# Kernel tuning notes

Hardware: AMD Instinct MI355X
Metric: run time of the kernel (lower is better)

Reference implementation:

```python
import jax, jax.numpy as jnp
import numpy as np

L, B, S, D = 4, 32, 512, 64  # labels, batch, seq_len (nodes), embed_dim
EDGE_P = 0.05                # adjacency density


def setup_inputs() -> dict:
    key = jax.random.key(0)
    ks = jax.random.split(key, 8)
    gcn_in = jax.random.normal(ks[0], (B, S, D), jnp.float32)
    # bool relational adjacency [L, B, S, S]; sparse-ish like real dependency/semantic graphs
    adj_mat = jax.random.bernoulli(ks[1], EDGE_P, (L, B, S, S))
    num_words = jnp.full((B,), float(S - 1), jnp.float32)
    eye = jnp.eye(D, dtype=jnp.float32)
    # weights initialized as identity (per tf.eye init) plus small noise so grads/outputs are non-trivial
    W_in = eye[None] + 0.05 * jax.random.normal(ks[2], (L, D, D), jnp.float32)
    W_out = eye[None] + 0.05 * jax.random.normal(ks[3], (L, D, D), jnp.float32)
    b_in = jnp.zeros((L, D), jnp.float32)
    b_out = jnp.zeros((L, D), jnp.float32)
    Wg_in = 0.05 * jax.random.normal(ks[4], (L, D), jnp.float32)
    Wg_out = 0.05 * jax.random.normal(ks[5], (L, D), jnp.float32)
    bg_in = jnp.zeros((L,), jnp.float32)
    bg_out = jnp.zeros((L,), jnp.float32)
    return {"gcn_in": gcn_in, "adj_mat": adj_mat, "num_words": num_words,
            "W_in": W_in, "b_in": b_in, "Wg_in": Wg_in, "bg_in": bg_in,
            "W_out": W_out, "b_out": b_out, "Wg_out": Wg_out, "bg_out": bg_out}


def reference(gcn_in, adj_mat, num_words, W_in, b_in, Wg_in, bg_in,
              W_out, b_out, Wg_out, bg_out):
    """RFGCN gcnLayer, 1 layer, aggregate='sum', w_gating=True, dropout off.

    All L relation labels are batched into single einsums instead of a
    Python loop over labels (same math, vectorized).
    """
    adj = adj_mat.astype(jnp.float32)  # [L,B,S,S], adj[l,b,src,dst]

    # self-loop: w_loop is a fixed identity -> loop_act == gcn_in
    act_sum = gcn_in  # [B,S,D]

    # ---- in-arcs: aggregate with adj^T (adj[l] transposed on last two dims) ----
    inp_in = jnp.einsum('bsd,lde->lbse', gcn_in, W_in) + b_in[:, None, None, :]
    # in_t[l,b,i] = sum_j adj[l,b,j,i] * inp_in[l,b,j]
    in_t = jnp.einsum('lbji,lbje->lbie', adj, inp_in)
    gin = jnp.einsum('bsd,ld->lbs', gcn_in, Wg_in) + bg_in[:, None, None]
    in_gate = jnp.einsum('lbji,lbj->lbi', adj, gin)
    in_act = in_t * jax.nn.sigmoid(in_gate)[..., None]

    # ---- out-arcs: aggregate with adj[l] directly ----
    inp_out = jnp.einsum('bsd,lde->lbse', gcn_in, W_out) + b_out[:, None, None, :]
    # out_t[l,b,i] = sum_j adj[l,b,i,j] * inp_out[l,b,j]
    out_t = jnp.einsum('lbij,lbje->lbie', adj, inp_out)
    gout = jnp.einsum('bsd,ld->lbs', gcn_in, Wg_out) + bg_out[:, None, None]
    out_gate = jnp.einsum('lbij,lbj->lbi', adj, gout)
    out_act = out_t * jax.nn.sigmoid(out_gate)[..., None]

    act_sum = act_sum + jnp.sum(in_act + out_act, axis=0)  # sum over labels
    act_sum = act_sum / (3.0 * num_words)[:, None, None]
    # single layer => last layer => no ReLU (relu applied only when layer != last)
    return act_sum
```

## Files before the change

### kernel.cpp

```cpp
#include <hip/hip_runtime.h>
#include <math.h>

typedef short short8 __attribute__((ext_vector_type(8)));
typedef float f32x4  __attribute__((ext_vector_type(4)));

constexpr int Ssz = 512, Dsz = 64, Lsz = 4, Bsz = 32;
constexpr int TI = 32, TJ = 64;

constexpr size_t XBF_OFF = 0;
constexpr size_t RM_OFF  = 2u * 1024 * 1024;
constexpr size_t CM_OFF  = RM_OFF + 4u * 1024 * 1024;
constexpr size_t WS_NEED = CM_OFF + 4u * 1024 * 1024;

constexpr int YBs = 69;
constexpr int YB_f = 0;
constexpr int WBs = 68;
constexpr int WB_f = YB_f + 32 * YBs;
constexpr int DG_f = WB_f + 64 * WBs;
constexpr int WG_f = DG_f + 32;
constexpr int BB_f = WG_f + 64;
constexpr int EPI_FLOATS = BB_f + 64;

__device__ __forceinline__ unsigned short f2bf(float x) {
    union { float f; unsigned u; } v; v.f = x;
    unsigned r = v.u + 0x7FFFu + ((v.u >> 16) & 1u);
    return (unsigned short)(r >> 16);
}

__global__ __launch_bounds__(256)
void xpose_kernel(const float* __restrict__ X, unsigned short* __restrict__ xbf)
{
    __shared__ unsigned short t[64][66];
    const int b = blockIdx.y, s0 = blockIdx.x * 64;
    const int tid = threadIdx.x;
    const int c = tid & 63, r4 = tid >> 6;
    const float* Xb = X + (size_t)b * Ssz * Dsz;
#pragma unroll
    for (int k = 0; k < 16; ++k) {
        const int s = r4 + 4 * k;
        t[s][c] = f2bf(Xb[(size_t)(s0 + s) * Dsz + c]);
    }
    __syncthreads();
    unsigned short* o = xbf + (size_t)b * Dsz * Ssz;
#pragma unroll
    for (int k = 0; k < 16; ++k) {
        const int d = r4 + 4 * k;
        o[(size_t)d * Ssz + s0 + c] = t[c][d];
    }
}

__global__ __launch_bounds__(256)
void mask_kernel(const int* __restrict__ adj,
                 unsigned long long* __restrict__ rm,
                 unsigned long long* __restrict__ cm)
{
    const int tid  = threadIdx.x;
    const int lane = tid & 63;
    const int wt   = blockIdx.x * 4 + (tid >> 6);
    const int lb   = wt >> 6;
    const int rem  = wt & 63;
    const int r1t  = (rem >> 3) * 64;
    const int r2t  = (rem & 7) * 64;
    const int* A = adj + (size_t)lb * Ssz * Ssz;

    unsigned long long c = 0ull, rmine = 0ull;
#pragma unroll 4
    for (int j = 0; j < 64; ++j) {
        const int a = A[(size_t)(r1t + j) * Ssz + r2t + lane];
        const unsigned long long bal = __ballot(a != 0);
        if (lane == j) rmine = bal;
        c |= ((unsigned long long)(a != 0)) << j;
    }
    rm[((size_t)lb * 8 + (r2t >> 6)) * 512 + r1t + lane] = rmine;
    cm[((size_t)lb * 8 + (r1t >> 6)) * 512 + r2t + lane] = c;
}

__global__ __launch_bounds__(512, 2)
void rfgcn_main(const float* __restrict__ X,
                const unsigned short* __restrict__ xbf,
                const unsigned long long* __restrict__ rm,
                const unsigned long long* __restrict__ cm,
                const float* __restrict__ nw,
                const float* __restrict__ W_in,  const float* __restrict__ b_in,
                const float* __restrict__ wg_in, const float* __restrict__ bg_in,
                const float* __restrict__ W_out, const float* __restrict__ b_out,
                const float* __restrict__ wg_out,const float* __restrict__ bg_out,
                float* __restrict__ out)
{
    __shared__ float smf[EPI_FLOATS];

    const int tid  = threadIdx.x;
    const int b    = blockIdx.y;
    const int i0   = blockIdx.x * TI;
    const int w    = tid >> 6;
    const int lane = tid & 63;
    const int dir  = w & 1;
    const int wl   = w >> 1;
    const int lm   = lane & 15;
    const int lg   = lane >> 4;

    f32x4 acc[2][4];
    f32x4 dacc[2];
#pragma unroll
    for (int rt = 0; rt < 2; ++rt) {
#pragma unroll
        for (int nt = 0; nt < 4; ++nt) acc[rt][nt] = (f32x4){0.f, 0.f, 0.f, 0.f};
        dacc[rt] = (f32x4){0.f, 0.f, 0.f, 0.f};
    }
    const short8 ones = {(short)0x3F80, (short)0x3F80, (short)0x3F80, (short)0x3F80,
                         (short)0x3F80, (short)0x3F80, (short)0x3F80, (short)0x3F80};

    const unsigned long long* Mb = (dir ? rm : cm) + (size_t)(wl * Bsz + b) * 8 * 512;
    const unsigned short* xp0 = xbf + (size_t)b * Dsz * Ssz;

    for (int jc = 0; jc < 8; ++jc) {
        const unsigned long long m0 = Mb[(size_t)jc * 512 + i0 + lm];
        const unsigned long long m1 = Mb[(size_t)jc * 512 + i0 + 16 + lm];
        const unsigned short* xp = xp0 + jc * 64;
#pragma unroll
        for (int ks = 0; ks < 2; ++ks) {
            short8 bh[4];
#pragma unroll
            for (int nt = 0; nt < 4; ++nt)
                bh[nt] = *(const short8*)(xp + (size_t)(16 * nt + lm) * Ssz + 8 * (4 * ks + lg));
#pragma unroll
            for (int rt = 0; rt < 2; ++rt) {
                const unsigned bytev = (unsigned)((rt ? m1 : m0) >> (32 * ks + 8 * lg)) & 0xFFu;
                short8 af;
#pragma unroll
                for (int jj = 0; jj < 8; ++jj)
                    af[jj] = ((bytev >> jj) & 1u) ? (short)0x3F80 : (short)0;
#pragma unroll
                for (int nt = 0; nt < 4; ++nt)
                    acc[rt][nt] = __builtin_amdgcn_mfma_f32_16x16x32_bf16(af, bh[nt], acc[rt][nt], 0, 0, 0);
                dacc[rt] = __builtin_amdgcn_mfma_f32_16x16x32_bf16(af, ones, dacc[rt], 0, 0, 0);
            }
        }
    }

    const int ei  = tid & 31;
    const int ecg = tid >> 5;
    float fin[4];
#pragma unroll
    for (int q = 0; q < 4; ++q) fin[q] = 0.f;

#pragma unroll
    for (int l = 0; l < Lsz; ++l) {
#pragma unroll
        for (int d2 = 0; d2 < 2; ++d2) {
            __syncthreads();
            if (dir == d2 && wl == l) {
#pragma unroll
                for (int rt = 0; rt < 2; ++rt)
#pragma unroll
                    for (int nt = 0; nt < 4; ++nt)
#pragma unroll
                        for (int r = 0; r < 4; ++r)
                            smf[YB_f + (16 * rt + 4 * lg + r) * YBs + nt * 16 + lm] = acc[rt][nt][r];
                if (lm == 0)
#pragma unroll
                    for (int rt = 0; rt < 2; ++rt)
#pragma unroll
                        for (int r = 0; r < 4; ++r)
                            smf[DG_f + 16 * rt + 4 * lg + r] = dacc[rt][r];
            }
            const float* Wp = (d2 ? W_out : W_in) + l * Dsz * Dsz;
            {
                const int r = tid >> 3, c8 = tid & 7;
                *(float4*)&smf[WB_f + r * WBs + 8 * c8]     = *(const float4*)&Wp[r * Dsz + 8 * c8];
                *(float4*)&smf[WB_f + r * WBs + 8 * c8 + 4] = *(const float4*)&Wp[r * Dsz + 8 * c8 + 4];
            }
            const float* wgp = (d2 ? wg_out : wg_in) + l * Dsz;
            const float* bp  = (d2 ? b_out  : b_in)  + l * Dsz;
            if (tid < 64)        smf[WG_f + tid]      = wgp[tid];
            else if (tid < 128)  smf[BB_f + tid - 64] = bp[tid - 64];
            const float bgs = (d2 ? bg_out : bg_in)[l];
            __syncthreads();

            const float dg = smf[DG_f + ei];
            float tq[4];
#pragma unroll
            for (int q = 0; q < 4; ++q) tq[q] = dg * smf[BB_f + 4 * ecg + q];
            float gate = dg * bgs;
#pragma unroll 4
            for (int e = 0; e < 64; ++e) {
                const float yv = smf[YB_f + ei * YBs + e];
                gate += yv * smf[WG_f + e];
#pragma unroll
                for (int q = 0; q < 4; ++q) tq[q] += yv * smf[WB_f + e * WBs + 4 * ecg + q];
            }
            const float sg = 1.f / (1.f + expf(-gate));
#pragma unroll
            for (int q = 0; q < 4; ++q) fin[q] += tq[q] * sg;
        }
    }

    const float inv = 1.f / (3.f * nw[b]);
    const float* Xb = X + (size_t)b * Ssz * Dsz;
    const float4 xr = *(const float4*)&Xb[(size_t)(i0 + ei) * Dsz + 4 * ecg];
    float4 o;
    o.x = (xr.x + fin[0]) * inv;
    o.y = (xr.y + fin[1]) * inv;
    o.z = (xr.z + fin[2]) * inv;
    o.w = (xr.w + fin[3]) * inv;
    *(float4*)(out + ((size_t)b * Ssz + i0 + ei) * Dsz + 4 * ecg) = o;
}

constexpr int XTb[2] = {0, 4096};
constexpr int FB_SMEM = EPI_FLOATS * 4;

__global__ __launch_bounds__(512, 4)
void rfgcn_fallback(const float* __restrict__ X, const int* __restrict__ adj,
                    const float* __restrict__ nw,
                    const float* __restrict__ W_in,  const float* __restrict__ b_in,
                    const float* __restrict__ wg_in, const float* __restrict__ bg_in,
                    const float* __restrict__ W_out, const float* __restrict__ b_out,
                    const float* __restrict__ wg_out,const float* __restrict__ bg_out,
                    float* __restrict__ out)
{
    __shared__ __align__(16) char smem[FB_SMEM];
    short* sm16 = (short*)smem;
    float* smf  = (float*)smem;

    const int tid  = threadIdx.x;
    const int b    = blockIdx.y;
    const int i0   = blockIdx.x * TI;
    const int w    = tid >> 6;
    const int lane = tid & 63;
    const int dir  = w & 1;
    const int wl   = w >> 1;
    const int lm   = lane & 15;
    const int lg   = lane >> 4;

    f32x4 acc[2][4];
    f32x4 dacc[2];
#pragma unroll
    for (int rt = 0; rt < 2; ++rt) {
#pragma unroll
        for (int nt = 0; nt < 4; ++nt) acc[rt][nt] = (f32x4){0.f, 0.f, 0.f, 0.f};
        dacc[rt] = (f32x4){0.f, 0.f, 0.f, 0.f};
    }
    const short8 ones = {(short)0x3F80, (short)0x3F80, (short)0x3F80, (short)0x3F80,
                         (short)0x3F80, (short)0x3F80, (short)0x3F80, (short)0x3F80};

    const float* Xb = X + (size_t)b * Ssz * Dsz;
    const int*   Ab = adj + ((size_t)wl * Bsz + b) * Ssz * Ssz;

    float xv[8];
    int   aR[32];

#define ADJ_LOAD(T)                                                              \
    {                                                                            \
        const int J0 = (T) * TJ;                                                 \
        if (dir == 0) {                                                          \
            _Pragma("unroll")                                                    \
            for (int rt = 0; rt < 2; ++rt)                                       \
                _Pragma("unroll")                                                \
                for (int ks = 0; ks < 2; ++ks)                                   \
                    _Pragma("unroll")                                            \
                    for (int j = 0; j < 8; ++j)                                  \
                        aR[rt * 16 + ks * 8 + j] =                               \
                            Ab[(size_t)(J0 + 32 * ks + 8 * lg + j) * Ssz + i0 + 16 * rt + lm]; \
        } else {                                                                 \
            _Pragma("unroll")                                                    \
            for (int rt = 0; rt < 2; ++rt)                                       \
                _Pragma("unroll")                                                \
                for (int ks = 0; ks < 2; ++ks) {                                 \
                    const int* p = &Ab[(size_t)(i0 + 16 * rt + lm) * Ssz + J0 + 32 * ks + 8 * lg]; \
                    const int4 q0 = *(const int4*)p;                             \
                    const int4 q1 = *(const int4*)(p + 4);                       \
                    aR[rt * 16 + ks * 8 + 0] = q0.x; aR[rt * 16 + ks * 8 + 1] = q0.y; \
                    aR[rt * 16 + ks * 8 + 2] = q0.z; aR[rt * 16 + ks * 8 + 3] = q0.w; \
                    aR[rt * 16 + ks * 8 + 4] = q1.x; aR[rt * 16 + ks * 8 + 5] = q1.y; \
                    aR[rt * 16 + ks * 8 + 6] = q1.z; aR[rt * 16 + ks * 8 + 7] = q1.w; \
                }                                                                \
        }                                                                        \
    }
#define X_LOAD(T)                                                                \
    {                                                                            \
        const int J0 = (T) * TJ;                                                 \
        _Pragma("unroll")                                                        \
        for (int s = 0; s < 8; ++s) xv[s] = Xb[(size_t)(J0 + 8 * w + s) * Dsz + lane]; \
    }
#define X_WRITE(BUF)                                                             \
    {                                                                            \
        short8 hi;                                                               \
        _Pragma("unroll")                                                        \
        for (int s = 0; s < 8; ++s) hi[s] = (short)f2bf(xv[s]);                  \
        const int g = w ^ (lane & 7);                                            \
        *(short8*)(sm16 + XTb[BUF] + lane * 64 + g * 8) = hi;                    \
    }

    X_LOAD(0)
    X_WRITE(0)
    ADJ_LOAD(0)
    X_LOAD(1)
    __syncthreads();

    for (int t = 0; t < 8; ++t) {
        const int cur = t & 1;
        short8 af[2][2];
#pragma unroll
        for (int rt = 0; rt < 2; ++rt)
#pragma unroll
            for (int ks = 0; ks < 2; ++ks)
#pragma unroll
                for (int j = 0; j < 8; ++j)
                    af[rt][ks][j] = aR[rt * 16 + ks * 8 + j] ? (short)0x3F80 : (short)0;

        if (t < 7) ADJ_LOAD(t + 1)
        if (t < 7) X_WRITE(cur ^ 1)
        if (t < 6) X_LOAD(t + 2)

#pragma unroll
        for (int ks = 0; ks < 2; ++ks) {
            short8 bh[4];
#pragma unroll
            for (int nt = 0; nt < 4; ++nt) {
                const int d = nt * 16 + lm;
                const int g = (4 * ks + lg) ^ (d & 7);
                bh[nt] = *(const short8*)(sm16 + XTb[cur] + d * 64 + g * 8);
            }
#pragma unroll
            for (int rt = 0; rt < 2; ++rt) {
#pragma unroll
                for (int nt = 0; nt < 4; ++nt)
                    acc[rt][nt] = __builtin_amdgcn_mfma_f32_16x16x32_bf16(af[rt][ks], bh[nt], acc[rt][nt], 0, 0, 0);
                dacc[rt] = __builtin_amdgcn_mfma_f32_16x16x32_bf16(af[rt][ks], ones, dacc[rt], 0, 0, 0);
            }
        }
        __syncthreads();
    }
#undef ADJ_LOAD
#undef X_LOAD
#undef X_WRITE

    const int ei  = tid & 31;
    const int ecg = tid >> 5;
    float fin[4];
#pragma unroll
    for (int q = 0; q < 4; ++q) fin[q] = 0.f;

#pragma unroll
    for (int l = 0; l < Lsz; ++l) {
#pragma unroll
        for (int d2 = 0; d2 < 2; ++d2) {
            if (l + d2) __syncthreads();
            if (dir == d2 && wl == l) {
#pragma unroll
                for (int rt = 0; rt < 2; ++rt)
#pragma unroll
                    for (int nt = 0; nt < 4; ++nt)
#pragma unroll
                        for (int r = 0; r < 4; ++r)
                            smf[YB_f + (16 * rt + 4 * lg + r) * YBs + nt * 16 + lm] = acc[rt][nt][r];
                if (lm == 0)
#pragma unroll
                    for (int rt = 0; rt < 2; ++rt)
#pragma unroll
                        for (int r = 0; r < 4; ++r)
                            smf[DG_f + 16 * rt + 4 * lg + r] = dacc[rt][r];
            }
            const float* Wp = (d2 ? W_out : W_in) + l * Dsz * Dsz;
            {
                const int r = tid >> 3, c8 = tid & 7;
                *(float4*)&smf[WB_f + r * WBs + 8 * c8]     = *(const float4*)&Wp[r * Dsz + 8 * c8];
                *(float4*)&smf[WB_f + r * WBs + 8 * c8 + 4] = *(const float4*)&Wp[r * Dsz + 8 * c8 + 4];
            }
            const float* wgp = (d2 ? wg_out : wg_in) + l * Dsz;
            const float* bp  = (d2 ? b_out  : b_in)  + l * Dsz;
            if (tid < 64)        smf[WG_f + tid]      = wgp[tid];
            else if (tid < 128)  smf[BB_f + tid - 64] = bp[tid - 64];
            const float bgs = (d2 ? bg_out : bg_in)[l];
            __syncthreads();

            const float dg = smf[DG_f + ei];
            float tq[4];
#pragma unroll
            for (int q = 0; q < 4; ++q) tq[q] = dg * smf[BB_f + 4 * ecg + q];
            float gate = dg * bgs;
#pragma unroll 4
            for (int e = 0; e < 64; ++e) {
                const float yv = smf[YB_f + ei * YBs + e];
                gate += yv * smf[WG_f + e];
#pragma unroll
                for (int q = 0; q < 4; ++q) tq[q] += yv * smf[WB_f + e * WBs + 4 * ecg + q];
            }
            const float sg = 1.f / (1.f + expf(-gate));
#pragma unroll
            for (int q = 0; q < 4; ++q) fin[q] += tq[q] * sg;
        }
    }

    const float inv = 1.f / (3.f * nw[b]);
    const float4 xr = *(const float4*)&Xb[(size_t)(i0 + ei) * Dsz + 4 * ecg];
    float4 o;
    o.x = (xr.x + fin[0]) * inv;
    o.y = (xr.y + fin[1]) * inv;
    o.z = (xr.z + fin[2]) * inv;
    o.w = (xr.w + fin[3]) * inv;
    *(float4*)(out + ((size_t)b * Ssz + i0 + ei) * Dsz + 4 * ecg) = o;
}

extern "C" void kernel_launch(void* const* d_in, const int* in_sizes, int n_in,
                              void* d_out, int out_size, void* d_ws, size_t ws_size,
                              hipStream_t stream)
{
    const float* X      = (const float*)d_in[0];
    const int*   adj    = (const int*)  d_in[1];
    const float* nw     = (const float*)d_in[2];
    const float* W_in   = (const float*)d_in[3];
    const float* b_in   = (const float*)d_in[4];
    const float* wg_in  = (const float*)d_in[5];
    const float* bg_in  = (const float*)d_in[6];
    const float* W_out  = (const float*)d_in[7];
    const float* b_out  = (const float*)d_in[8];
    const float* wg_out = (const float*)d_in[9];
    const float* bg_out = (const float*)d_in[10];
    float* out = (float*)d_out;

    if (ws_size >= WS_NEED) {
        unsigned short*      xbf = (unsigned short*)((char*)d_ws + XBF_OFF);
        unsigned long long*  rmp = (unsigned long long*)((char*)d_ws + RM_OFF);
        unsigned long long*  cmp = (unsigned long long*)((char*)d_ws + CM_OFF);
        hipLaunchKernelGGL(xpose_kernel, dim3(8, 32), dim3(256), 0, stream, X, xbf);
        hipLaunchKernelGGL(mask_kernel, dim3(2048), dim3(256), 0, stream, adj, rmp, cmp);
        hipLaunchKernelGGL(rfgcn_main, dim3(Ssz / TI, Bsz), dim3(512), 0, stream,
                           X, xbf, rmp, cmp, nw, W_in, b_in, wg_in, bg_in,
                           W_out, b_out, wg_out, bg_out, out);
    } else {
        hipLaunchKernelGGL(rfgcn_fallback, dim3(Ssz / TI, Bsz), dim3(512), 0, stream,
                           X, adj, nw, W_in, b_in, wg_in, bg_in,
                           W_out, b_out, wg_out, bg_out, out);
    }
}
```

Baseline: 92.07 us.

## Run per-label epilogue projection on MFMA in parallel across warps

The epilogue used to loop serially over the 8 (label, direction) pairs, with a block-wide sync and a scalar FP32 64x64 projection for each. Now every warp stages its own aggregated tile as bf16 in swizzled LDS and projects it with MFMA against bf16-converted W, with the gate weights as an extra column tile. Results are summed into a shared buffer through LDS atomics. This removes 16 barriers and the scalar FMA loop, and launch bounds are raised to 4 blocks per CU, at the cost of rounding the intermediate and the weights to bf16 and reading weights uncoalesced from global memory.

```diff
diff --git a/kernel.cpp b/kernel.cpp
--- a/kernel.cpp
+++ b/kernel.cpp
@@ -11,6 +11,11 @@
 constexpr size_t RM_OFF  = 2u * 1024 * 1024;
 constexpr size_t CM_OFF  = RM_OFF + 4u * 1024 * 1024;
 constexpr size_t WS_NEED = CM_OFF + 4u * 1024 * 1024;
+
+constexpr int YS_B   = 0;
+constexpr int DEG_B2 = 32768;
+constexpr int FIN_B2 = DEG_B2 + 1024;
+constexpr int MAIN_SMEM = FIN_B2 + 8448;
 
 constexpr int YBs = 69;
 constexpr int YB_f = 0;
@@ -75,7 +80,7 @@
     cm[((size_t)lb * 8 + (r1t >> 6)) * 512 + r2t + lane] = c;
 }
 
-__global__ __launch_bounds__(512, 2)
+__global__ __launch_bounds__(512, 4)
 void rfgcn_main(const float* __restrict__ X,
                 const unsigned short* __restrict__ xbf,
                 const unsigned long long* __restrict__ rm,
@@ -87,7 +92,10 @@
                 const float* __restrict__ wg_out,const float* __restrict__ bg_out,
                 float* __restrict__ out)
 {
-    __shared__ float smf[EPI_FLOATS];
+    __shared__ __align__(16) char smem[MAIN_SMEM];
+    short* sm16 = (short*)smem;
+    float* degf = (float*)(smem + DEG_B2);
+    float* finf = (float*)(smem + FIN_B2);
 
     const int tid  = threadIdx.x;
     const int b    = blockIdx.y;
@@ -99,6 +107,8 @@
     const int lm   = lane & 15;
     const int lg   = lane >> 4;
 
+    for (int k = tid; k < 64 * 33; k += 512) finf[k] = 0.f;
+
     f32x4 acc[2][4];
     f32x4 dacc[2];
 #pragma unroll
@@ -138,72 +148,103 @@
         }
     }
 
-    const int ei  = tid & 31;
-    const int ecg = tid >> 5;
-    float fin[4];
-#pragma unroll
-    for (int q = 0; q < 4; ++q) fin[q] = 0.f;
-
-#pragma unroll
-    for (int l = 0; l < Lsz; ++l) {
-#pragma unroll
-        for (int d2 = 0; d2 < 2; ++d2) {
-            __syncthreads();
-            if (dir == d2 && wl == l) {
-#pragma unroll
-                for (int rt = 0; rt < 2; ++rt)
-#pragma unroll
-                    for (int nt = 0; nt < 4; ++nt)
-#pragma unroll
-                        for (int r = 0; r < 4; ++r)
-                            smf[YB_f + (16 * rt + 4 * lg + r) * YBs + nt * 16 + lm] = acc[rt][nt][r];
-                if (lm == 0)
-#pragma unroll
-                    for (int rt = 0; rt < 2; ++rt)
-#pragma unroll
-                        for (int r = 0; r < 4; ++r)
-                            smf[DG_f + 16 * rt + 4 * lg + r] = dacc[rt][r];
-            }
-            const float* Wp = (d2 ? W_out : W_in) + l * Dsz * Dsz;
-            {
-                const int r = tid >> 3, c8 = tid & 7;
-                *(float4*)&smf[WB_f + r * WBs + 8 * c8]     = *(const float4*)&Wp[r * Dsz + 8 * c8];
-                *(float4*)&smf[WB_f + r * WBs + 8 * c8 + 4] = *(const float4*)&Wp[r * Dsz + 8 * c8 + 4];
-            }
-            const float* wgp = (d2 ? wg_out : wg_in) + l * Dsz;
-            const float* bp  = (d2 ? b_out  : b_in)  + l * Dsz;
-            if (tid < 64)        smf[WG_f + tid]      = wgp[tid];
-            else if (tid < 128)  smf[BB_f + tid - 64] = bp[tid - 64];
-            const float bgs = (d2 ? bg_out : bg_in)[l];
-            __syncthreads();
-
-            const float dg = smf[DG_f + ei];
-            float tq[4];
-#pragma unroll
-            for (int q = 0; q < 4; ++q) tq[q] = dg * smf[BB_f + 4 * ecg + q];
-            float gate = dg * bgs;
-#pragma unroll 4
-            for (int e = 0; e < 64; ++e) {
-                const float yv = smf[YB_f + ei * YBs + e];
-                gate += yv * smf[WG_f + e];
-#pragma unroll
-                for (int q = 0; q < 4; ++q) tq[q] += yv * smf[WB_f + e * WBs + 4 * ecg + q];
-            }
-            const float sg = 1.f / (1.f + expf(-gate));
-#pragma unroll
-            for (int q = 0; q < 4; ++q) fin[q] += tq[q] * sg;
-        }
-    }
+    short* Ys = sm16 + YS_B / 2 + w * 2048;
+#pragma unroll
+    for (int rt = 0; rt < 2; ++rt)
+#pragma unroll
+        for (int nt = 0; nt < 4; ++nt)
+#pragma unroll
+            for (int r = 0; r < 4; ++r) {
+                const int row = 16 * rt + 4 * lg + r;
+                const int gs  = (((2 * nt + (lm >> 3)) ^ (row & 7)) << 3) + (lm & 7);
+                Ys[row * 64 + gs] = (short)f2bf(acc[rt][nt][r]);
+            }
+    if (lm == 0) {
+#pragma unroll
+        for (int rt = 0; rt < 2; ++rt)
+#pragma unroll
+            for (int r = 0; r < 4; ++r)
+                degf[w * 32 + 16 * rt + 4 * lg + r] = dacc[rt][r];
+    }
+
+    short8 by[2][2];
+#pragma unroll
+    for (int it = 0; it < 2; ++it)
+#pragma unroll
+        for (int ks = 0; ks < 2; ++ks) {
+            const int i  = 16 * it + lm;
+            const int gs = ((lg + 4 * ks) ^ (i & 7)) << 3;
+            by[it][ks] = *(const short8*)(Ys + i * 64 + gs);
+        }
+    float degv[2];
+#pragma unroll
+    for (int it = 0; it < 2; ++it) degv[it] = degf[w * 32 + 16 * it + lm];
+
+    const float* Wp  = (dir ? W_out  : W_in)  + wl * Dsz * Dsz;
+    const float* wgp = (dir ? wg_out : wg_in) + wl * Dsz;
+    const float* bp  = (dir ? b_out  : b_in)  + wl * Dsz;
+    const float  bgv = (dir ? bg_out : bg_in)[wl];
+
+    f32x4 accT[5][2];
+#pragma unroll
+    for (int ct = 0; ct < 5; ++ct)
+#pragma unroll
+        for (int it = 0; it < 2; ++it) accT[ct][it] = (f32x4){0.f, 0.f, 0.f, 0.f};
+
+#pragma unroll
+    for (int ct = 0; ct < 5; ++ct) {
+#pragma unroll
+        for (int ks = 0; ks < 2; ++ks) {
+            short8 aw;
+            if (ct < 4) {
+                const int c = 16 * ct + lm;
+#pragma unroll
+                for (int j = 0; j < 8; ++j)
+                    aw[j] = (short)f2bf(Wp[(size_t)(8 * lg + j + 32 * ks) * Dsz + c]);
+            } else {
+#pragma unroll
+                for (int j = 0; j < 8; ++j)
+                    aw[j] = (short)f2bf(wgp[8 * lg + j + 32 * ks]);
+            }
+#pragma unroll
+            for (int it = 0; it < 2; ++it)
+                accT[ct][it] = __builtin_amdgcn_mfma_f32_16x16x32_bf16(aw, by[it][ks], accT[ct][it], 0, 0, 0);
+        }
+    }
+
+    float sg[2];
+#pragma unroll
+    for (int it = 0; it < 2; ++it) {
+        const float g = accT[4][it][0] + degv[it] * bgv;
+        sg[it] = 1.f / (1.f + expf(-g));
+    }
+    __syncthreads();
+#pragma unroll
+    for (int ct = 0; ct < 4; ++ct)
+#pragma unroll
+        for (int r = 0; r < 4; ++r) {
+            const int c = 16 * ct + 4 * lg + r;
+            const float bc = bp[c];
+#pragma unroll
+            for (int it = 0; it < 2; ++it) {
+                const float v = (accT[ct][it][r] + degv[it] * bc) * sg[it];
+                atomicAdd(&finf[c * 33 + 16 * it + lm], v);
+            }
+        }
+
+    __syncthreads();
 
     const float inv = 1.f / (3.f * nw[b]);
     const float* Xb = X + (size_t)b * Ssz * Dsz;
-    const float4 xr = *(const float4*)&Xb[(size_t)(i0 + ei) * Dsz + 4 * ecg];
+    const int oi = tid >> 4;
+    const int c4 = (tid & 15) * 4;
+    const float4 xv = *(const float4*)&Xb[(size_t)(i0 + oi) * Dsz + c4];
     float4 o;
-    o.x = (xr.x + fin[0]) * inv;
-    o.y = (xr.y + fin[1]) * inv;
-    o.z = (xr.z + fin[2]) * inv;
-    o.w = (xr.w + fin[3]) * inv;
-    *(float4*)(out + ((size_t)b * Ssz + i0 + ei) * Dsz + 4 * ecg) = o;
+    o.x = (xv.x + finf[(c4 + 0) * 33 + oi]) * inv;
+    o.y = (xv.y + finf[(c4 + 1) * 33 + oi]) * inv;
+    o.z = (xv.z + finf[(c4 + 2) * 33 + oi]) * inv;
+    o.w = (xv.w + finf[(c4 + 3) * 33 + oi]) * inv;
+    *(float4*)(out + ((size_t)b * Ssz + i0 + oi) * Dsz + c4) = o;
 }
 
 constexpr int XTb[2] = {0, 4096};
```

Result: slower. 108.7 us (+18.1%).

## Split fused aggregation/epilogue kernel into separate MFMA aggregation and epilogue kernels

Applied to the files above, without the earlier changes.

The fused main kernel is split in two. A 64-thread agg_kernel, launched per (tile, batch, label*direction), computes the masked aggregation and degree with MFMA and writes them to a global workspace. A separate epi_kernel then streams each aggregate into LDS and applies the weight projection, gating and sum. The aim is more independent blocks for the aggregation phase and lighter epilogue blocks with higher occupancy. In exchange, roughly 32MB of intermediate fp32 data makes a round trip through global memory, and there is one more kernel launch.

```diff
diff --git a/kernel.cpp b/kernel.cpp
--- a/kernel.cpp
+++ b/kernel.cpp
@@ -8,9 +8,11 @@
 constexpr int TI = 32, TJ = 64;
 
 constexpr size_t XBF_OFF = 0;
-constexpr size_t RM_OFF  = 2u * 1024 * 1024;
-constexpr size_t CM_OFF  = RM_OFF + 4u * 1024 * 1024;
-constexpr size_t WS_NEED = CM_OFF + 4u * 1024 * 1024;
+constexpr size_t RM_OFF  = 2u  * 1024 * 1024;
+constexpr size_t CM_OFF  = 6u  * 1024 * 1024;
+constexpr size_t Y_OFF   = 10u * 1024 * 1024;
+constexpr size_t D_OFF   = 42u * 1024 * 1024;
+constexpr size_t WS_NEED = D_OFF + 512u * 1024;
 
 constexpr int YBs = 69;
 constexpr int YB_f = 0;
@@ -75,11 +77,81 @@
     cm[((size_t)lb * 8 + (r1t >> 6)) * 512 + r2t + lane] = c;
 }
 
-__global__ __launch_bounds__(512, 2)
-void rfgcn_main(const float* __restrict__ X,
-                const unsigned short* __restrict__ xbf,
+__global__ __launch_bounds__(64, 4)
+void agg_kernel(const unsigned short* __restrict__ xbf,
                 const unsigned long long* __restrict__ rm,
                 const unsigned long long* __restrict__ cm,
+                float* __restrict__ Yws, float* __restrict__ Dws)
+{
+    const int ix   = blockIdx.x;
+    const int b    = blockIdx.y;
+    const int dirl = blockIdx.z;
+    const int dir  = dirl & 1, wl = dirl >> 1;
+    const int lane = threadIdx.x;
+    const int lm   = lane & 15;
+    const int lg   = lane >> 4;
+    const int i0   = ix * TI;
+
+    f32x4 acc[2][4];
+    f32x4 dacc[2];
+#pragma unroll
+    for (int rt = 0; rt < 2; ++rt) {
+#pragma unroll
+        for (int nt = 0; nt < 4; ++nt) acc[rt][nt] = (f32x4){0.f, 0.f, 0.f, 0.f};
+        dacc[rt] = (f32x4){0.f, 0.f, 0.f, 0.f};
+    }
+    const short8 ones = {(short)0x3F80, (short)0x3F80, (short)0x3F80, (short)0x3F80,
+                         (short)0x3F80, (short)0x3F80, (short)0x3F80, (short)0x3F80};
+
+    const unsigned long long* Mb = (dir ? rm : cm) + (size_t)(wl * Bsz + b) * 8 * 512;
+    const unsigned short* xp0 = xbf + (size_t)b * Dsz * Ssz;
+
+    for (int jc = 0; jc < 8; ++jc) {
+        const unsigned long long m0 = Mb[(size_t)jc * 512 + i0 + lm];
+        const unsigned long long m1 = Mb[(size_t)jc * 512 + i0 + 16 + lm];
+        const unsigned short* xp = xp0 + jc * 64;
+#pragma unroll
+        for (int ks = 0; ks < 2; ++ks) {
+            short8 bh[4];
+#pragma unroll
+            for (int nt = 0; nt < 4; ++nt)
+                bh[nt] = *(const short8*)(xp + (size_t)(16 * nt + lm) * Ssz + 8 * (4 * ks + lg));
+#pragma unroll
+            for (int rt = 0; rt < 2; ++rt) {
+                const unsigned bytev = (unsigned)((rt ? m1 : m0) >> (32 * ks + 8 * lg)) & 0xFFu;
+                short8 af;
+#pragma unroll
+                for (int jj = 0; jj < 8; ++jj)
+                    af[jj] = ((bytev >> jj) & 1u) ? (short)0x3F80 : (short)0;
+#pragma unroll
+                for (int nt = 0; nt < 4; ++nt)
+                    acc[rt][nt] = __builtin_amdgcn_mfma_f32_16x16x32_bf16(af, bh[nt], acc[rt][nt], 0, 0, 0);
+                dacc[rt] = __builtin_amdgcn_mfma_f32_16x16x32_bf16(af, ones, dacc[rt], 0, 0, 0);
+            }
+        }
+    }
+
+    float* Yp = Yws + ((size_t)dirl * Bsz + b) * Ssz * Dsz;
+#pragma unroll
+    for (int rt = 0; rt < 2; ++rt)
+#pragma unroll
+        for (int nt = 0; nt < 4; ++nt)
+#pragma unroll
+            for (int r = 0; r < 4; ++r)
+                Yp[(size_t)(i0 + 16 * rt + 4 * lg + r) * Dsz + 16 * nt + lm] = acc[rt][nt][r];
+    if (lm == 0) {
+        float* Dp = Dws + ((size_t)dirl * Bsz + b) * Ssz;
+#pragma unroll
+        for (int rt = 0; rt < 2; ++rt)
+#pragma unroll
+            for (int r = 0; r < 4; ++r)
+                Dp[i0 + 16 * rt + 4 * lg + r] = dacc[rt][r];
+    }
+}
+
+__global__ __launch_bounds__(512, 4)
+void epi_kernel(const float* __restrict__ X,
+                const float* __restrict__ Yws, const float* __restrict__ Dws,
                 const float* __restrict__ nw,
                 const float* __restrict__ W_in,  const float* __restrict__ b_in,
                 const float* __restrict__ wg_in, const float* __restrict__ bg_in,
@@ -88,56 +160,9 @@
                 float* __restrict__ out)
 {
     __shared__ float smf[EPI_FLOATS];
-
-    const int tid  = threadIdx.x;
-    const int b    = blockIdx.y;
-    const int i0   = blockIdx.x * TI;
-    const int w    = tid >> 6;
-    const int lane = tid & 63;
-    const int dir  = w & 1;
-    const int wl   = w >> 1;
-    const int lm   = lane & 15;
-    const int lg   = lane >> 4;
-
-    f32x4 acc[2][4];
-    f32x4 dacc[2];
-#pragma unroll
-    for (int rt = 0; rt < 2; ++rt) {
-#pragma unroll
-        for (int nt = 0; nt < 4; ++nt) acc[rt][nt] = (f32x4){0.f, 0.f, 0.f, 0.f};
-        dacc[rt] = (f32x4){0.f, 0.f, 0.f, 0.f};
-    }
-    const short8 ones = {(short)0x3F80, (short)0x3F80, (short)0x3F80, (short)0x3F80,
-                         (short)0x3F80, (short)0x3F80, (short)0x3F80, (short)0x3F80};
-
-    const unsigned long long* Mb = (dir ? rm : cm) + (size_t)(wl * Bsz + b) * 8 * 512;
-    const unsigned short* xp0 = xbf + (size_t)b * Dsz * Ssz;
-
-    for (int jc = 0; jc < 8; ++jc) {
-        const unsigned long long m0 = Mb[(size_t)jc * 512 + i0 + lm];
-        const unsigned long long m1 = Mb[(size_t)jc * 512 + i0 + 16 + lm];
-        const unsigned short* xp = xp0 + jc * 64;
-#pragma unroll
-        for (int ks = 0; ks < 2; ++ks) {
-            short8 bh[4];
-#pragma unroll
-            for (int nt = 0; nt < 4; ++nt)
-                bh[nt] = *(const short8*)(xp + (size_t)(16 * nt + lm) * Ssz + 8 * (4 * ks + lg));
-#pragma unroll
-            for (int rt = 0; rt < 2; ++rt) {
-                const unsigned bytev = (unsigned)((rt ? m1 : m0) >> (32 * ks + 8 * lg)) & 0xFFu;
-                short8 af;
-#pragma unroll
-                for (int jj = 0; jj < 8; ++jj)
-                    af[jj] = ((bytev >> jj) & 1u) ? (short)0x3F80 : (short)0;
-#pragma unroll
-                for (int nt = 0; nt < 4; ++nt)
-                    acc[rt][nt] = __builtin_amdgcn_mfma_f32_16x16x32_bf16(af, bh[nt], acc[rt][nt], 0, 0, 0);
-                dacc[rt] = __builtin_amdgcn_mfma_f32_16x16x32_bf16(af, ones, dacc[rt], 0, 0, 0);
-            }
-        }
-    }
-
+    const int tid = threadIdx.x;
+    const int b   = blockIdx.y;
+    const int i0  = blockIdx.x * TI;
     const int ei  = tid & 31;
     const int ecg = tid >> 5;
     float fin[4];
@@ -148,22 +173,19 @@
     for (int l = 0; l < Lsz; ++l) {
 #pragma unroll
         for (int d2 = 0; d2 < 2; ++d2) {
-            __syncthreads();
-            if (dir == d2 && wl == l) {
-#pragma unroll
-                for (int rt = 0; rt < 2; ++rt)
-#pragma unroll
-                    for (int nt = 0; nt < 4; ++nt)
-#pragma unroll
-                        for (int r = 0; r < 4; ++r)
-                            smf[YB_f + (16 * rt + 4 * lg + r) * YBs + nt * 16 + lm] = acc[rt][nt][r];
-                if (lm == 0)
-#pragma unroll
-                    for (int rt = 0; rt < 2; ++rt)
-#pragma unroll
-                        for (int r = 0; r < 4; ++r)
-                            smf[DG_f + 16 * rt + 4 * lg + r] = dacc[rt][r];
-            }
+            if (l + d2) __syncthreads();
+            {
+                const float* Yp = Yws + ((size_t)(2 * l + d2) * Bsz + b) * Ssz * Dsz
+                                + (size_t)i0 * Dsz;
+                const float4 yv = *(const float4*)&Yp[tid * 4];
+                const int row = tid >> 4, col = (tid & 15) * 4;
+                smf[YB_f + row * YBs + col + 0] = yv.x;
+                smf[YB_f + row * YBs + col + 1] = yv.y;
+                smf[YB_f + row * YBs + col + 2] = yv.z;
+                smf[YB_f + row * YBs + col + 3] = yv.w;
+            }
+            if (tid < 32)
+                smf[DG_f + tid] = Dws[((size_t)(2 * l + d2) * Bsz + b) * Ssz + i0 + tid];
             const float* Wp = (d2 ? W_out : W_in) + l * Dsz * Dsz;
             {
                 const int r = tid >> 3, c8 = tid & 7;
@@ -172,8 +194,8 @@
             }
             const float* wgp = (d2 ? wg_out : wg_in) + l * Dsz;
             const float* bp  = (d2 ? b_out  : b_in)  + l * Dsz;
-            if (tid < 64)        smf[WG_f + tid]      = wgp[tid];
-            else if (tid < 128)  smf[BB_f + tid - 64] = bp[tid - 64];
+            if (tid >= 384 && tid < 448)      smf[WG_f + tid - 384] = wgp[tid - 384];
+            else if (tid >= 448)              smf[BB_f + tid - 448] = bp[tid - 448];
             const float bgs = (d2 ? bg_out : bg_in)[l];
             __syncthreads();
 
@@ -420,13 +442,17 @@
     float* out = (float*)d_out;
 
     if (ws_size >= WS_NEED) {
-        unsigned short*      xbf = (unsigned short*)((char*)d_ws + XBF_OFF);
-        unsigned long long*  rmp = (unsigned long long*)((char*)d_ws + RM_OFF);
-        unsigned long long*  cmp = (unsigned long long*)((char*)d_ws + CM_OFF);
+        unsigned short*     xbf = (unsigned short*)((char*)d_ws + XBF_OFF);
+        unsigned long long* rmp = (unsigned long long*)((char*)d_ws + RM_OFF);
+        unsigned long long* cmp = (unsigned long long*)((char*)d_ws + CM_OFF);
+        float*              Yws = (float*)((char*)d_ws + Y_OFF);
+        float*              Dws = (float*)((char*)d_ws + D_OFF);
         hipLaunchKernelGGL(xpose_kernel, dim3(8, 32), dim3(256), 0, stream, X, xbf);
         hipLaunchKernelGGL(mask_kernel, dim3(2048), dim3(256), 0, stream, adj, rmp, cmp);
-        hipLaunchKernelGGL(rfgcn_main, dim3(Ssz / TI, Bsz), dim3(512), 0, stream,
-                           X, xbf, rmp, cmp, nw, W_in, b_in, wg_in, bg_in,
+        hipLaunchKernelGGL(agg_kernel, dim3(16, 32, 8), dim3(64), 0, stream,
+                           xbf, rmp, cmp, Yws, Dws);
+        hipLaunchKernelGGL(epi_kernel, dim3(16, 32), dim3(512), 0, stream,
+                           X, Yws, Dws, nw, W_in, b_in, wg_in, bg_in,
                            W_out, b_out, wg_out, bg_out, out);
     } else {
         hipLaunchKernelGGL(rfgcn_fallback, dim3(Ssz / TI, Bsz), dim3(512), 0, stream,
```

New measurement: 105.7 us. 14.8% more time.
